# Optimization experiments

Measured on AMD Instinct MI355X. Metric: run time of the kernel, lower is better.

The kernel has to match this reference:

```python
import jax, jax.numpy as jnp
import numpy as np

B, C, H, W = 32, 512, 64, 64
RED = 16
HID = C // RED


def setup_inputs() -> dict:
    key = jax.random.key(0)
    ks = jax.random.split(key, 10)
    s1 = 1.0 / np.sqrt(C)
    s2 = 1.0 / np.sqrt(HID)
    return {
        "x": jax.random.normal(ks[0], (B, C, H, W), dtype=jnp.float32),
        # mlp_avg: Linear(C->HID), Linear(HID->C); torch convention W:[out,in]
        "Wa1": jax.random.uniform(ks[1], (HID, C), jnp.float32, -s1, s1),
        "ba1": jax.random.uniform(ks[2], (HID,), jnp.float32, -s1, s1),
        "Wa2": jax.random.uniform(ks[3], (C, HID), jnp.float32, -s2, s2),
        "ba2": jax.random.uniform(ks[4], (C,), jnp.float32, -s2, s2),
        # mlp_max
        "Wm1": jax.random.uniform(ks[5], (HID, C), jnp.float32, -s1, s1),
        "bm1": jax.random.uniform(ks[6], (HID,), jnp.float32, -s1, s1),
        "Wm2": jax.random.uniform(ks[7], (C, HID), jnp.float32, -s2, s2),
        "bm2": jax.random.uniform(ks[8], (C,), jnp.float32, -s2, s2),
        "fusion_w": jax.random.normal(ks[9], (5, 1), dtype=jnp.float32),
    }


def reference(x, Wa1, ba1, Wa2, ba2, Wm1, bm1, Wm2, bm2, fusion_w):
    b, c, h, w = x.shape
    hs, ws = h // 2, w // 2

    def mlp(v, W1, b1, W2, b2):  # v: [..., c]
        return jax.nn.relu(v @ W1.T + b1) @ W2.T + b2

    # quadrant view: [b, c, 2, hs, 2, ws]; quadrant (i,j) == x[:,:,i*hs:(i+1)*hs, j*ws:(j+1)*ws]
    xq = x.reshape(b, c, 2, hs, 2, ws)
    avg_q = xq.mean(axis=(3, 5))          # [b, c, 2, 2]
    max_q = xq.max(axis=(3, 5))           # [b, c, 2, 2]
    avg_g = x.mean(axis=(2, 3))           # [b, c]
    max_g = x.max(axis=(2, 3))            # [b, c]

    # stack regions in order [global, x1=(0,0), x2=(0,1), x3=(1,0), x4=(1,1)] -> [5, b, c]
    avg_all = jnp.concatenate(
        [avg_g[None], avg_q.transpose(2, 3, 0, 1).reshape(4, b, c)], axis=0)
    max_all = jnp.concatenate(
        [max_g[None], max_q.transpose(2, 3, 0, 1).reshape(4, b, c)], axis=0)

    feats = mlp(avg_all, Wa1, ba1, Wa2, ba2) + mlp(max_all, Wm1, bm1, Wm2, bm2)  # [5, b, c]

    fw = jax.nn.softmax(fusion_w[:, 0], axis=0)          # [5]
    fused = jnp.einsum('sbc,s->bc', feats, fw)           # [b, c]

    global_att = jax.nn.sigmoid(fused)                   # [b, c]
    local_att = jax.nn.sigmoid(feats[1:])                # [4, b, c] (x1..x4)
    scale = local_att + global_att[None]                 # [4, b, c]

    # scatter per-quadrant scale back into [b, c, 2, 1, 2, 1] and multiply
    s = scale.reshape(2, 2, b, c).transpose(2, 3, 0, 1)[:, :, :, None, :, None]
    out = (xq * s).reshape(b, c, h, w)
    return out
```

## Files before the change

### kernel.cpp

```cpp
#include <hip/hip_runtime.h>
#include <math.h>

#define Bn  32
#define Cn  512
#define HIDn 32
#define BCn (Bn*Cn)

typedef float f32x4 __attribute__((ext_vector_type(4)));

__global__ __launch_bounds__(256) void stats_kernel(const float* __restrict__ x,
                                                    float* __restrict__ avg_all,
                                                    float* __restrict__ max_all) {
  const int plane = blockIdx.x;
  const float4* xp = (const float4*)(x + (size_t)plane * 4096);
  const int tid = threadIdx.x;

  float sTop = 0.f, sBot = 0.f;
  float mTop = -INFINITY, mBot = -INFINITY;
#pragma unroll
  for (int k = 0; k < 4; ++k) {
    float4 v = xp[tid + k * 256];
    float s = (v.x + v.y) + (v.z + v.w);
    float m = fmaxf(fmaxf(v.x, v.y), fmaxf(v.z, v.w));
    if (k < 2) { sTop += s; mTop = fmaxf(mTop, m); }
    else       { sBot += s; mBot = fmaxf(mBot, m); }
  }
  const int jside = ((tid & 15) >= 8) ? 1 : 0;

  float qs[4] = {0.f, 0.f, 0.f, 0.f};
  float qm[4] = {-INFINITY, -INFINITY, -INFINITY, -INFINITY};
  qs[jside]     = sTop; qm[jside]     = mTop;
  qs[2 + jside] = sBot; qm[2 + jside] = mBot;

#pragma unroll
  for (int off = 32; off > 0; off >>= 1) {
#pragma unroll
    for (int q = 0; q < 4; ++q) {
      qs[q] += __shfl_down(qs[q], off);
      qm[q] = fmaxf(qm[q], __shfl_down(qm[q], off));
    }
  }

  __shared__ float ls[4][4], lm[4][4];
  const int wave = tid >> 6;
  if ((tid & 63) == 0) {
#pragma unroll
    for (int q = 0; q < 4; ++q) { ls[wave][q] = qs[q]; lm[wave][q] = qm[q]; }
  }
  __syncthreads();
  if (tid == 0) {
    float gsum = 0.f, gmax = -INFINITY;
#pragma unroll
    for (int q = 0; q < 4; ++q) {
      float s = (ls[0][q] + ls[1][q]) + (ls[2][q] + ls[3][q]);
      float m = fmaxf(fmaxf(lm[0][q], lm[1][q]), fmaxf(lm[2][q], lm[3][q]));
      avg_all[(1 + q) * BCn + plane] = s * (1.f / 1024.f);
      max_all[(1 + q) * BCn + plane] = m;
      gsum += s; gmax = fmaxf(gmax, m);
    }
    avg_all[plane] = gsum * (1.f / 4096.f);
    max_all[plane] = gmax;
  }
}

__global__ __launch_bounds__(256) void mlp_kernel(
    const float* __restrict__ avg_all, const float* __restrict__ max_all,
    const float* __restrict__ Wa1, const float* __restrict__ ba1,
    const float* __restrict__ Wa2, const float* __restrict__ ba2,
    const float* __restrict__ Wm1, const float* __restrict__ bm1,
    const float* __restrict__ Wm2, const float* __restrict__ bm2,
    const float* __restrict__ fusion_w, float* __restrict__ scale_ws) {
  const int b = blockIdx.x;
  const int tid = threadIdx.x;

  __shared__ __align__(16) float s_v[2][5][Cn];
  __shared__ float s_h[2][5][HIDn];

  for (int i = tid; i < 5 * Cn; i += 256) {
    int s = i >> 9, c = i & (Cn - 1);
    s_v[0][s][c] = avg_all[s * BCn + b * Cn + c];
    s_v[1][s][c] = max_all[s * BCn + b * Cn + c];
  }
  __syncthreads();

  for (int d = tid; d < 2 * 5 * HIDn; d += 256) {
    int mlp = d / 160, r = d % 160;
    int s = r >> 5, k = r & 31;
    const float* W1 = mlp ? Wm1 : Wa1;
    const float* b1 = mlp ? bm1 : ba1;
    const float4* wrow = (const float4*)(W1 + k * Cn);
    const float4* v = (const float4*)s_v[mlp][s];
    float acc = b1[k];
    for (int c4 = 0; c4 < Cn / 4; ++c4) {
      float4 w = wrow[c4], xv = v[c4];
      acc += w.x * xv.x + w.y * xv.y + w.z * xv.z + w.w * xv.w;
    }
    s_h[mlp][s][k] = fmaxf(acc, 0.f);
  }
  __syncthreads();

  float fw[5]; float fmx = -INFINITY;
#pragma unroll
  for (int s = 0; s < 5; ++s) { fw[s] = fusion_w[s]; fmx = fmaxf(fmx, fw[s]); }
  float fsum = 0.f;
#pragma unroll
  for (int s = 0; s < 5; ++s) { fw[s] = expf(fw[s] - fmx); fsum += fw[s]; }
  const float finv = 1.f / fsum;

  {
    const int c = blockIdx.y * 256 + tid;
    const float* wa = Wa2 + c * HIDn;
    const float* wm = Wm2 + c * HIDn;
    const float bias = ba2[c] + bm2[c];
    float f[5];
#pragma unroll
    for (int s = 0; s < 5; ++s) {
      float acc = bias;
#pragma unroll
      for (int k = 0; k < HIDn; ++k)
        acc += wa[k] * s_h[0][s][k] + wm[k] * s_h[1][s][k];
      f[s] = acc;
    }
    float fused = 0.f;
#pragma unroll
    for (int s = 0; s < 5; ++s) fused += fw[s] * f[s];
    fused *= finv;
    const float g = 1.f / (1.f + expf(-fused));
    float4 sc;
    sc.x = 1.f / (1.f + expf(-f[1])) + g;
    sc.y = 1.f / (1.f + expf(-f[2])) + g;
    sc.z = 1.f / (1.f + expf(-f[3])) + g;
    sc.w = 1.f / (1.f + expf(-f[4])) + g;
    ((float4*)scale_ws)[b * Cn + c] = sc;
  }
}

__global__ __launch_bounds__(256) void apply_kernel(const float* __restrict__ x,
                                                    const float* __restrict__ scale_ws,
                                                    float* __restrict__ out) {
  const int plane = blockIdx.x;
  const int tid = threadIdx.x;
  const f32x4* xp = (const f32x4*)(x + (size_t)plane * 4096);
  f32x4* op = (f32x4*)(out + (size_t)plane * 4096);

  const float4 sc = ((const float4*)scale_ws)[plane];
  const float s[4] = {sc.x, sc.y, sc.z, sc.w};
  const int jside = ((tid & 15) >= 8) ? 1 : 0;

#pragma unroll
  for (int k = 0; k < 4; ++k) {
    const float m = s[((k < 2) ? 0 : 2) + jside];
    f32x4 v = xp[tid + k * 256];
    v *= m;
    __builtin_nontemporal_store(v, &op[tid + k * 256]);
  }
}

extern "C" void kernel_launch(void* const* d_in, const int* in_sizes, int n_in,
                              void* d_out, int out_size, void* d_ws, size_t ws_size,
                              hipStream_t stream) {
  const float* x        = (const float*)d_in[0];
  const float* Wa1      = (const float*)d_in[1];
  const float* ba1      = (const float*)d_in[2];
  const float* Wa2      = (const float*)d_in[3];
  const float* ba2      = (const float*)d_in[4];
  const float* Wm1      = (const float*)d_in[5];
  const float* bm1      = (const float*)d_in[6];
  const float* Wm2      = (const float*)d_in[7];
  const float* bm2      = (const float*)d_in[8];
  const float* fusion_w = (const float*)d_in[9];
  float* out = (float*)d_out;

  float* ws       = (float*)d_ws;
  float* avg_all  = ws;
  float* max_all  = ws + 5 * BCn;
  float* scale_ws = ws + 10 * BCn;

  stats_kernel<<<BCn, 256, 0, stream>>>(x, avg_all, max_all);
  mlp_kernel<<<dim3(Bn, 2), 256, 0, stream>>>(avg_all, max_all,
                                              Wa1, ba1, Wa2, ba2,
                                              Wm1, bm1, Wm2, bm2,
                                              fusion_w, scale_ws);
  apply_kernel<<<BCn, 256, 0, stream>>>(x, scale_ws, out);
}
```

Baseline: 183.7 us.

## Map one wavefront per plane in stats and apply kernels

```diff
diff --git a/kernel.cpp b/kernel.cpp
--- a/kernel.cpp
+++ b/kernel.cpp
@@ -11,55 +11,44 @@
 __global__ __launch_bounds__(256) void stats_kernel(const float* __restrict__ x,
                                                     float* __restrict__ avg_all,
                                                     float* __restrict__ max_all) {
-  const int plane = blockIdx.x;
-  const float4* xp = (const float4*)(x + (size_t)plane * 4096);
-  const int tid = threadIdx.x;
+  const int wave = threadIdx.x >> 6;
+  const int lane = threadIdx.x & 63;
+  const int plane = blockIdx.x * 4 + wave;
+  const f32x4* xp = (const f32x4*)(x + (size_t)plane * 4096);
 
-  float sTop = 0.f, sBot = 0.f;
-  float mTop = -INFINITY, mBot = -INFINITY;
+  float sT = 0.f, sB = 0.f, mT = -INFINITY, mB = -INFINITY;
 #pragma unroll
-  for (int k = 0; k < 4; ++k) {
-    float4 v = xp[tid + k * 256];
+  for (int i = 0; i < 16; ++i) {
+    f32x4 v = xp[lane + 64 * i];
     float s = (v.x + v.y) + (v.z + v.w);
     float m = fmaxf(fmaxf(v.x, v.y), fmaxf(v.z, v.w));
-    if (k < 2) { sTop += s; mTop = fmaxf(mTop, m); }
-    else       { sBot += s; mBot = fmaxf(mBot, m); }
-  }
-  const int jside = ((tid & 15) >= 8) ? 1 : 0;
-
-  float qs[4] = {0.f, 0.f, 0.f, 0.f};
-  float qm[4] = {-INFINITY, -INFINITY, -INFINITY, -INFINITY};
-  qs[jside]     = sTop; qm[jside]     = mTop;
-  qs[2 + jside] = sBot; qm[2 + jside] = mBot;
-
-#pragma unroll
-  for (int off = 32; off > 0; off >>= 1) {
-#pragma unroll
-    for (int q = 0; q < 4; ++q) {
-      qs[q] += __shfl_down(qs[q], off);
-      qm[q] = fmaxf(qm[q], __shfl_down(qm[q], off));
-    }
+    if (i < 8) { sT += s; mT = fmaxf(mT, m); }
+    else       { sB += s; mB = fmaxf(mB, m); }
   }
 
-  __shared__ float ls[4][4], lm[4][4];
-  const int wave = tid >> 6;
-  if ((tid & 63) == 0) {
+  const int masks[5] = {1, 2, 4, 16, 32};
 #pragma unroll
-    for (int q = 0; q < 4; ++q) { ls[wave][q] = qs[q]; lm[wave][q] = qm[q]; }
+  for (int t = 0; t < 5; ++t) {
+    const int msk = masks[t];
+    sT += __shfl_xor(sT, msk);
+    sB += __shfl_xor(sB, msk);
+    mT = fmaxf(mT, __shfl_xor(mT, msk));
+    mB = fmaxf(mB, __shfl_xor(mB, msk));
   }
-  __syncthreads();
-  if (tid == 0) {
-    float gsum = 0.f, gmax = -INFINITY;
-#pragma unroll
-    for (int q = 0; q < 4; ++q) {
-      float s = (ls[0][q] + ls[1][q]) + (ls[2][q] + ls[3][q]);
-      float m = fmaxf(fmaxf(lm[0][q], lm[1][q]), fmaxf(lm[2][q], lm[3][q]));
-      avg_all[(1 + q) * BCn + plane] = s * (1.f / 1024.f);
-      max_all[(1 + q) * BCn + plane] = m;
-      gsum += s; gmax = fmaxf(gmax, m);
-    }
-    avg_all[plane] = gsum * (1.f / 4096.f);
-    max_all[plane] = gmax;
+  const float sTo = __shfl_xor(sT, 8), sBo = __shfl_xor(sB, 8);
+  const float mTo = __shfl_xor(mT, 8), mBo = __shfl_xor(mB, 8);
+
+  if (lane == 0) {
+    avg_all[1 * BCn + plane] = sT  * (1.f / 1024.f);
+    avg_all[2 * BCn + plane] = sTo * (1.f / 1024.f);
+    avg_all[3 * BCn + plane] = sB  * (1.f / 1024.f);
+    avg_all[4 * BCn + plane] = sBo * (1.f / 1024.f);
+    avg_all[plane]           = (sT + sTo + sB + sBo) * (1.f / 4096.f);
+    max_all[1 * BCn + plane] = mT;
+    max_all[2 * BCn + plane] = mTo;
+    max_all[3 * BCn + plane] = mB;
+    max_all[4 * BCn + plane] = mBo;
+    max_all[plane]           = fmaxf(fmaxf(mT, mTo), fmaxf(mB, mBo));
   }
 }
 
@@ -88,11 +77,11 @@
     int s = r >> 5, k = r & 31;
     const float* W1 = mlp ? Wm1 : Wa1;
     const float* b1 = mlp ? bm1 : ba1;
-    const float4* wrow = (const float4*)(W1 + k * Cn);
-    const float4* v = (const float4*)s_v[mlp][s];
+    const f32x4* wrow = (const f32x4*)(W1 + k * Cn);
+    const f32x4* v = (const f32x4*)s_v[mlp][s];
     float acc = b1[k];
     for (int c4 = 0; c4 < Cn / 4; ++c4) {
-      float4 w = wrow[c4], xv = v[c4];
+      f32x4 w = wrow[c4], xv = v[c4];
       acc += w.x * xv.x + w.y * xv.y + w.z * xv.z + w.w * xv.w;
     }
     s_h[mlp][s][k] = fmaxf(acc, 0.f);
@@ -138,21 +127,22 @@
 __global__ __launch_bounds__(256) void apply_kernel(const float* __restrict__ x,
                                                     const float* __restrict__ scale_ws,
                                                     float* __restrict__ out) {
-  const int plane = blockIdx.x;
-  const int tid = threadIdx.x;
+  const int wave = threadIdx.x >> 6;
+  const int lane = threadIdx.x & 63;
+  const int plane = blockIdx.x * 4 + wave;
+  const int jside = ((lane & 15) >= 8) ? 1 : 0;
+
+  const float scT = scale_ws[plane * 4 + jside];
+  const float scB = scale_ws[plane * 4 + 2 + jside];
+
   const f32x4* xp = (const f32x4*)(x + (size_t)plane * 4096);
   f32x4* op = (f32x4*)(out + (size_t)plane * 4096);
 
-  const float4 sc = ((const float4*)scale_ws)[plane];
-  const float s[4] = {sc.x, sc.y, sc.z, sc.w};
-  const int jside = ((tid & 15) >= 8) ? 1 : 0;
-
 #pragma unroll
-  for (int k = 0; k < 4; ++k) {
-    const float m = s[((k < 2) ? 0 : 2) + jside];
-    f32x4 v = xp[tid + k * 256];
-    v *= m;
-    __builtin_nontemporal_store(v, &op[tid + k * 256]);
+  for (int i = 0; i < 16; ++i) {
+    f32x4 v = __builtin_nontemporal_load(&xp[lane + 64 * i]);
+    v *= (i < 8) ? scT : scB;
+    __builtin_nontemporal_store(v, &op[lane + 64 * i]);
   }
 }
 
@@ -176,10 +166,10 @@
   float* max_all  = ws + 5 * BCn;
   float* scale_ws = ws + 10 * BCn;
 
-  stats_kernel<<<BCn, 256, 0, stream>>>(x, avg_all, max_all);
+  stats_kernel<<<BCn / 4, 256, 0, stream>>>(x, avg_all, max_all);
   mlp_kernel<<<dim3(Bn, 2), 256, 0, stream>>>(avg_all, max_all,
                                               Wa1, ba1, Wa2, ba2,
                                               Wm1, bm1, Wm2, bm2,
                                               fusion_w, scale_ws);
-  apply_kernel<<<BCn, 256, 0, stream>>>(x, scale_ws, out);
+  apply_kernel<<<BCn / 4, 256, 0, stream>>>(x, scale_ws, out);
 }
```

Result: faster. 161.5 us (-12.1%).
